# Kernel optimization log

Measured on AMD Instinct MI355X. Metric: run time of the kernel, lower is better.

Reference implementation:

```python
import jax, jax.numpy as jnp
import numpy as np

HID, HEADS = 1024, 16
HEAD_DIM = HID // HEADS
B, S = 4, 2048


def setup_inputs() -> dict:
    key = jax.random.key(0)
    ks = jax.random.split(key, 12)
    scale = 0.02
    inp = {
        "query": jax.random.normal(ks[0], (B, S, HID), jnp.float32),
        "key_in": jax.random.normal(ks[1], (B, S, HID), jnp.float32),
        "value": jax.random.normal(ks[2], (B, S, HID), jnp.float32),
        "mask": jnp.ones((B, 1, 1, S), jnp.int32),
        "Wq": jax.random.normal(ks[3], (HID, HID), jnp.float32) * scale,
        "bq": jnp.zeros((HID,), jnp.float32),
        "Wk": jax.random.normal(ks[4], (HID, HID), jnp.float32) * scale,
        "bk": jnp.zeros((HID,), jnp.float32),
        "Wv": jax.random.normal(ks[5], (HID, HID), jnp.float32) * scale,
        "bv": jnp.zeros((HID,), jnp.float32),
        "Wo": jax.random.normal(ks[6], (HID, HID), jnp.float32) * scale,
        "bo": jnp.zeros((HID,), jnp.float32),
    }
    return inp


def reference(query, key_in, value, mask, Wq, bq, Wk, bk, Wv, bv, Wo, bo):
    # Linear projections (torch Linear: x @ W.T + b)
    Q = query @ Wq.T + bq
    K = key_in @ Wk.T + bk
    V = value @ Wv.T + bv
    # [B, H, S, Dh]
    def split_heads(x):
        return x.reshape(B, -1, HEADS, HEAD_DIM).transpose(0, 2, 1, 3)
    Q, K, V = split_heads(Q), split_heads(K), split_heads(V)
    scale = jnp.sqrt(jnp.float32(HEAD_DIM))
    # multiplicative (scaled dot-product) attention: [B,H,Sq,Sk]
    energy = jnp.einsum("bhqd,bhkd->bhqk", Q, K) / scale
    energy = jnp.where(mask == 0, jnp.float32(-1e10), energy)
    attention = jax.nn.softmax(energy, axis=-1)
    x = jnp.einsum("bhqk,bhkd->bhqd", attention, V)  # dropout p=0
    x = x.transpose(0, 2, 1, 3).reshape(B, -1, HID)
    x = x @ Wo.T + bo
    return (x, attention)
```

## Files before the change

kernel.cpp:

```cpp
#include <hip/hip_runtime.h>
#include <hip/hip_bf16.h>
#include <stdint.h>
#include <stddef.h>

#define HID    1024
#define NHEADS 16
#define HD     64
#define BATCH  4
#define SEQ    2048

typedef __attribute__((ext_vector_type(8))) short short8;
typedef __attribute__((ext_vector_type(4))) short short4v;
typedef __attribute__((ext_vector_type(4))) float float4v;

static __device__ __forceinline__ short f2bf(float f) {
    unsigned u = __builtin_bit_cast(unsigned, f);
    u += 0x7fffu + ((u >> 16) & 1u);
    return (short)(u >> 16);
}

__global__ __launch_bounds__(256) void cvt_f32_bf16(const float* __restrict__ in,
                                                    short* __restrict__ out, int n4) {
    int i = blockIdx.x * 256 + threadIdx.x;
    if (i < n4) {
        float4v v = ((const float4v*)in)[i];
        short4v o;
        o[0] = f2bf(v[0]); o[1] = f2bf(v[1]); o[2] = f2bf(v[2]); o[3] = f2bf(v[3]);
        ((short4v*)out)[i] = o;
    }
}

template<int MODE, bool A_BF16>
__global__ __launch_bounds__(256) void gemm_kernel(const void* __restrict__ Aptr,
                                                   const short* __restrict__ Wb,
                                                   const float* __restrict__ bias,
                                                   void* __restrict__ outp) {
    const int lane = threadIdx.x & 63;
    const int w    = threadIdx.x >> 6;
    const int l15  = lane & 15;
    const int quad = lane >> 4;
    const int m0   = blockIdx.x * 64 + w * 16;
    const int n0   = blockIdx.y * 128;

    float4v acc[8];
#pragma unroll
    for (int i = 0; i < 8; i++)
#pragma unroll
        for (int j = 0; j < 4; j++) acc[i][j] = 0.0f;

    const int arow = m0 + l15;
    for (int ks = 0; ks < 1024; ks += 32) {
        const int koff = ks + quad * 8;
        short8 af;
        if (A_BF16) {
            const short* Ab = (const short*)Aptr;
            af = *(const short8*)(Ab + (size_t)arow * 1024 + koff);
        } else {
            const float* Af = (const float*)Aptr;
            float4v a0 = *(const float4v*)(Af + (size_t)arow * 1024 + koff);
            float4v a1 = *(const float4v*)(Af + (size_t)arow * 1024 + koff + 4);
            af[0] = f2bf(a0[0]); af[1] = f2bf(a0[1]); af[2] = f2bf(a0[2]); af[3] = f2bf(a0[3]);
            af[4] = f2bf(a1[0]); af[5] = f2bf(a1[1]); af[6] = f2bf(a1[2]); af[7] = f2bf(a1[3]);
        }
#pragma unroll
        for (int ns = 0; ns < 8; ns++) {
            const short8 bf = *(const short8*)(Wb + (size_t)(n0 + ns * 16 + l15) * 1024 + koff);
            acc[ns] = __builtin_amdgcn_mfma_f32_16x16x32_bf16(af, bf, acc[ns], 0, 0, 0);
        }
    }

#pragma unroll
    for (int ns = 0; ns < 8; ns++) {
        const int n = n0 + ns * 16 + l15;
        const float bv = bias[n];
        if (MODE == 0) {
            short* outb = (short*)outp;
#pragma unroll
            for (int r = 0; r < 4; r++) {
                const int m = m0 + quad * 4 + r;
                outb[(size_t)m * 1024 + n] = f2bf(acc[ns][r] + bv);
            }
        } else if (MODE == 1) {
            short* outb = (short*)outp;
            const int mb = m0 + quad * 4;
            const int b_ = mb >> 11, s_ = mb & 2047;
            const int h_ = n >> 6,  d_ = n & 63;
            short4v pk;
#pragma unroll
            for (int r = 0; r < 4; r++) pk[r] = f2bf(acc[ns][r] + bv);
            *(short4v*)(outb + ((size_t)((b_ * NHEADS + h_) * HD + d_)) * SEQ + s_) = pk;
        } else {
            float* outf = (float*)outp;
#pragma unroll
            for (int r = 0; r < 4; r++) {
                const int m = m0 + quad * 4 + r;
                outf[(size_t)m * 1024 + n] = acc[ns][r] + bv;
            }
        }
    }
}

__global__ __launch_bounds__(256) void attn_kernel(const short* __restrict__ Q,
                                                   const short* __restrict__ K,
                                                   const short* __restrict__ Vt,
                                                   const int* __restrict__ mask,
                                                   float* __restrict__ attn_out,
                                                   short* __restrict__ Xattn) {
    __shared__ short sP[4][16][40];

    const int lane = threadIdx.x & 63;
    const int w    = threadIdx.x >> 6;
    const int l15  = lane & 15;
    const int quad = lane >> 4;
    const int qblk = blockIdx.x & 31;
    const int bh   = blockIdx.x >> 5;
    const int b    = bh >> 4;
    const int h    = bh & 15;
    const int q0   = qblk * 64 + w * 16;

    const short* Qrow = Q + ((size_t)(b * SEQ + q0 + l15) * HID) + h * HD;
    const short8 aq0 = *(const short8*)(Qrow + quad * 8);
    const short8 aq1 = *(const short8*)(Qrow + 32 + quad * 8);

    const short* Kb   = K + (size_t)(b * SEQ) * HID + h * HD;
    const int*   mrow = mask + b * SEQ;
    const float  scale = 0.125f;

    float rs[4] = {0.f, 0.f, 0.f, 0.f};
    for (int n0 = 0; n0 < SEQ; n0 += 16) {
        const short* kr = Kb + (size_t)(n0 + l15) * HID + quad * 8;
        const short8 bk0 = *(const short8*)kr;
        const short8 bk1 = *(const short8*)(kr + 32);
        float4v e;
#pragma unroll
        for (int j = 0; j < 4; j++) e[j] = 0.0f;
        e = __builtin_amdgcn_mfma_f32_16x16x32_bf16(aq0, bk0, e, 0, 0, 0);
        e = __builtin_amdgcn_mfma_f32_16x16x32_bf16(aq1, bk1, e, 0, 0, 0);
        const int mv = mrow[n0 + l15];
#pragma unroll
        for (int r = 0; r < 4; r++) {
            float x = e[r] * scale;
            x = mv ? x : -1e10f;
            rs[r] += __expf(x);
        }
    }
#pragma unroll
    for (int r = 0; r < 4; r++) {
        float s = rs[r];
        s += __shfl_xor(s, 1, 64);
        s += __shfl_xor(s, 2, 64);
        s += __shfl_xor(s, 4, 64);
        s += __shfl_xor(s, 8, 64);
        rs[r] = 1.0f / s;
    }

    float4v oacc[4];
#pragma unroll
    for (int i = 0; i < 4; i++)
#pragma unroll
        for (int j = 0; j < 4; j++) oacc[i][j] = 0.0f;

    float* pout = attn_out + (size_t)(bh * SEQ + q0) * SEQ;
    const short* Vb = Vt + (size_t)bh * HD * SEQ;

    for (int n0 = 0; n0 < SEQ; n0 += 32) {
#pragma unroll
        for (int ns = 0; ns < 2; ns++) {
            const int nn = n0 + ns * 16;
            const short* kr = Kb + (size_t)(nn + l15) * HID + quad * 8;
            const short8 bk0 = *(const short8*)kr;
            const short8 bk1 = *(const short8*)(kr + 32);
            float4v e;
#pragma unroll
            for (int j = 0; j < 4; j++) e[j] = 0.0f;
            e = __builtin_amdgcn_mfma_f32_16x16x32_bf16(aq0, bk0, e, 0, 0, 0);
            e = __builtin_amdgcn_mfma_f32_16x16x32_bf16(aq1, bk1, e, 0, 0, 0);
            const int mv = mrow[nn + l15];
#pragma unroll
            for (int r = 0; r < 4; r++) {
                float x = e[r] * scale;
                x = mv ? x : -1e10f;
                const float p = __expf(x) * rs[r];
                const int m = quad * 4 + r;
                pout[(size_t)m * SEQ + nn + l15] = p;
                sP[w][m][ns * 16 + l15] = f2bf(p);
            }
        }
        __syncthreads();
        const short8 ap = *(const short8*)(&sP[w][l15][quad * 8]);
#pragma unroll
        for (int dn = 0; dn < 4; dn++) {
            const short8 bv = *(const short8*)(Vb + (size_t)(dn * 16 + l15) * SEQ + n0 + quad * 8);
            oacc[dn] = __builtin_amdgcn_mfma_f32_16x16x32_bf16(ap, bv, oacc[dn], 0, 0, 0);
        }
        __syncthreads();
    }

#pragma unroll
    for (int dn = 0; dn < 4; dn++)
#pragma unroll
        for (int r = 0; r < 4; r++) {
            const int m = quad * 4 + r;
            Xattn[(size_t)(b * SEQ + q0 + m) * HID + h * HD + dn * 16 + l15] = f2bf(oacc[dn][r]);
        }
}

extern "C" void kernel_launch(void* const* d_in, const int* in_sizes, int n_in,
                              void* d_out, int out_size, void* d_ws, size_t ws_size,
                              hipStream_t stream) {
    const float* query  = (const float*)d_in[0];
    const float* key_in = (const float*)d_in[1];
    const float* value  = (const float*)d_in[2];
    const int*   mask   = (const int*)d_in[3];
    const float* Wq = (const float*)d_in[4];
    const float* bq = (const float*)d_in[5];
    const float* Wk = (const float*)d_in[6];
    const float* bk = (const float*)d_in[7];
    const float* Wv = (const float*)d_in[8];
    const float* bv = (const float*)d_in[9];
    const float* Wo = (const float*)d_in[10];
    const float* bo = (const float*)d_in[11];

    char* ws = (char*)d_ws;
    const size_t MiB = 1024 * 1024;
    short* Wq_b = (short*)(ws + 0 * MiB);
    short* Wk_b = (short*)(ws + 2 * MiB);
    short* Wv_b = (short*)(ws + 4 * MiB);
    short* Wo_b = (short*)(ws + 6 * MiB);
    short* Qw   = (short*)(ws + 8 * MiB);
    short* Kw   = (short*)(ws + 24 * MiB);
    short* Vtw  = (short*)(ws + 40 * MiB);
    short* Xa   = (short*)(ws + 56 * MiB);

    const int wn4 = HID * HID / 4;
    cvt_f32_bf16<<<wn4 / 256, 256, 0, stream>>>(Wq, Wq_b, wn4);
    cvt_f32_bf16<<<wn4 / 256, 256, 0, stream>>>(Wk, Wk_b, wn4);
    cvt_f32_bf16<<<wn4 / 256, 256, 0, stream>>>(Wv, Wv_b, wn4);
    cvt_f32_bf16<<<wn4 / 256, 256, 0, stream>>>(Wo, Wo_b, wn4);

    dim3 gg(BATCH * SEQ / 64, HID / 128);
    gemm_kernel<0, false><<<gg, 256, 0, stream>>>(query,  Wq_b, bq, Qw);
    gemm_kernel<0, false><<<gg, 256, 0, stream>>>(key_in, Wk_b, bk, Kw);
    gemm_kernel<1, false><<<gg, 256, 0, stream>>>(value,  Wv_b, bv, Vtw);

    float* attn_out = (float*)d_out + (size_t)BATCH * SEQ * HID;
    attn_kernel<<<BATCH * NHEADS * (SEQ / 64), 256, 0, stream>>>(Qw, Kw, Vtw, mask, attn_out, Xa);

    gemm_kernel<2, true><<<gg, 256, 0, stream>>>(Xa, Wo_b, bo, d_out);
}
```

Baseline: 2.318 ms.

## Tile GEMMs through LDS, store Q/K head-major, prefetch K in attention

Replaces the register-only projection GEMM with a 128x128 LDS-tiled kernel. Tiles are filled by direct global-to-LDS loads, and block ids are swizzled for cache locality. Activations are first converted to bf16 in a separate pass, reusing a scratch buffer. Q and K are now written head-major so attention reads contiguous 64-element rows, and the attention loops software-prefetch the next K tile. Block barriers in the PV loop are replaced by a waitcnt, since each warp only uses its own sP slice. The cost is extra conversion kernels and an unpipelined single LDS buffer.

```diff
diff --git a/kernel.cpp b/kernel.cpp
--- a/kernel.cpp
+++ b/kernel.cpp
@@ -1,5 +1,4 @@
 #include <hip/hip_runtime.h>
-#include <hip/hip_bf16.h>
 #include <stdint.h>
 #include <stddef.h>
 
@@ -18,6 +17,11 @@
     u += 0x7fffu + ((u >> 16) & 1u);
     return (short)(u >> 16);
 }
+
+#define GLD_LDS16(g, l)                                        \
+    __builtin_amdgcn_global_load_lds(                          \
+        (__attribute__((address_space(1))) void*)(g),          \
+        (__attribute__((address_space(3))) void*)(l), 16, 0, 0)
 
 __global__ __launch_bounds__(256) void cvt_f32_bf16(const float* __restrict__ in,
                                                     short* __restrict__ out, int n4) {
@@ -30,71 +34,96 @@
     }
 }
 
-template<int MODE, bool A_BF16>
-__global__ __launch_bounds__(256) void gemm_kernel(const void* __restrict__ Aptr,
-                                                   const short* __restrict__ Wb,
-                                                   const float* __restrict__ bias,
-                                                   void* __restrict__ outp) {
-    const int lane = threadIdx.x & 63;
-    const int w    = threadIdx.x >> 6;
+template<int MODE>
+__global__ __launch_bounds__(256) void gemm_bf16(const short* __restrict__ A,
+                                                 const short* __restrict__ Wb,
+                                                 const float* __restrict__ bias,
+                                                 void* __restrict__ outp) {
+    __shared__ short As[128 * 32];
+    __shared__ short Bs[128 * 32];
+
+    const int id = blockIdx.x;
+    const int xt = (id & 7) * 8 + ((id >> 3) & 7);
+    const int yt = id >> 6;
+    const int m0 = xt * 128;
+    const int n0 = yt * 128;
+
+    const int t    = threadIdx.x;
+    const int lane = t & 63;
+    const int w    = t >> 6;
     const int l15  = lane & 15;
     const int quad = lane >> 4;
-    const int m0   = blockIdx.x * 64 + w * 16;
-    const int n0   = blockIdx.y * 128;
-
-    float4v acc[8];
-#pragma unroll
-    for (int i = 0; i < 8; i++)
-#pragma unroll
-        for (int j = 0; j < 4; j++) acc[i][j] = 0.0f;
-
-    const int arow = m0 + l15;
+    const int wm   = (w >> 1) * 64;
+    const int wn   = (w & 1) * 64;
+
+    float4v acc[4][4];
+#pragma unroll
+    for (int i = 0; i < 4; i++)
+#pragma unroll
+        for (int j = 0; j < 4; j++)
+#pragma unroll
+            for (int r = 0; r < 4; r++) acc[i][j][r] = 0.0f;
+
+    const int tr = t >> 2;
+    const int tc = (t & 3) * 8;
+    const short* Ag = A  + (size_t)(m0 + tr) * 1024 + tc;
+    const short* Wg = Wb + (size_t)(n0 + tr) * 1024 + tc;
+    short* a_dst = As + t * 8;
+    short* b_dst = Bs + t * 8;
+
     for (int ks = 0; ks < 1024; ks += 32) {
-        const int koff = ks + quad * 8;
-        short8 af;
-        if (A_BF16) {
-            const short* Ab = (const short*)Aptr;
-            af = *(const short8*)(Ab + (size_t)arow * 1024 + koff);
-        } else {
-            const float* Af = (const float*)Aptr;
-            float4v a0 = *(const float4v*)(Af + (size_t)arow * 1024 + koff);
-            float4v a1 = *(const float4v*)(Af + (size_t)arow * 1024 + koff + 4);
-            af[0] = f2bf(a0[0]); af[1] = f2bf(a0[1]); af[2] = f2bf(a0[2]); af[3] = f2bf(a0[3]);
-            af[4] = f2bf(a1[0]); af[5] = f2bf(a1[1]); af[6] = f2bf(a1[2]); af[7] = f2bf(a1[3]);
-        }
-#pragma unroll
-        for (int ns = 0; ns < 8; ns++) {
-            const short8 bf = *(const short8*)(Wb + (size_t)(n0 + ns * 16 + l15) * 1024 + koff);
-            acc[ns] = __builtin_amdgcn_mfma_f32_16x16x32_bf16(af, bf, acc[ns], 0, 0, 0);
-        }
-    }
-
-#pragma unroll
-    for (int ns = 0; ns < 8; ns++) {
-        const int n = n0 + ns * 16 + l15;
+        __syncthreads();
+        GLD_LDS16(Ag + ks,             a_dst);
+        GLD_LDS16(Ag + 64 * 1024 + ks, a_dst + 2048);
+        GLD_LDS16(Wg + ks,             b_dst);
+        GLD_LDS16(Wg + 64 * 1024 + ks, b_dst + 2048);
+        __syncthreads();
+
+        short8 af[4], bfr[4];
+#pragma unroll
+        for (int mi = 0; mi < 4; mi++)
+            af[mi] = *(const short8*)(As + (wm + mi * 16 + l15) * 32 + quad * 8);
+#pragma unroll
+        for (int ni = 0; ni < 4; ni++)
+            bfr[ni] = *(const short8*)(Bs + (wn + ni * 16 + l15) * 32 + quad * 8);
+#pragma unroll
+        for (int mi = 0; mi < 4; mi++)
+#pragma unroll
+            for (int ni = 0; ni < 4; ni++)
+                acc[mi][ni] = __builtin_amdgcn_mfma_f32_16x16x32_bf16(
+                    af[mi], bfr[ni], acc[mi][ni], 0, 0, 0);
+    }
+
+#pragma unroll
+    for (int ni = 0; ni < 4; ni++) {
+        const int n = n0 + wn + ni * 16 + l15;
         const float bv = bias[n];
-        if (MODE == 0) {
-            short* outb = (short*)outp;
-#pragma unroll
-            for (int r = 0; r < 4; r++) {
-                const int m = m0 + quad * 4 + r;
-                outb[(size_t)m * 1024 + n] = f2bf(acc[ns][r] + bv);
-            }
-        } else if (MODE == 1) {
-            short* outb = (short*)outp;
-            const int mb = m0 + quad * 4;
-            const int b_ = mb >> 11, s_ = mb & 2047;
-            const int h_ = n >> 6,  d_ = n & 63;
-            short4v pk;
-#pragma unroll
-            for (int r = 0; r < 4; r++) pk[r] = f2bf(acc[ns][r] + bv);
-            *(short4v*)(outb + ((size_t)((b_ * NHEADS + h_) * HD + d_)) * SEQ + s_) = pk;
-        } else {
-            float* outf = (float*)outp;
-#pragma unroll
-            for (int r = 0; r < 4; r++) {
-                const int m = m0 + quad * 4 + r;
-                outf[(size_t)m * 1024 + n] = acc[ns][r] + bv;
+#pragma unroll
+        for (int mi = 0; mi < 4; mi++) {
+            const int mb = m0 + wm + mi * 16 + quad * 4;
+            if (MODE == 3) {
+                short* ob = (short*)outp;
+                const int h_ = n >> 6, d_ = n & 63;
+                const int b_ = mb >> 11;
+#pragma unroll
+                for (int r = 0; r < 4; r++) {
+                    const int s_ = (mb + r) & 2047;
+                    ob[((size_t)(b_ * NHEADS + h_) * SEQ + s_) * HD + d_] =
+                        f2bf(acc[mi][ni][r] + bv);
+                }
+            } else if (MODE == 1) {
+                short* ob = (short*)outp;
+                const int h_ = n >> 6, d_ = n & 63;
+                const int b_ = mb >> 11, s_ = mb & 2047;
+                short4v pk;
+#pragma unroll
+                for (int r = 0; r < 4; r++) pk[r] = f2bf(acc[mi][ni][r] + bv);
+                *(short4v*)(ob + ((size_t)((b_ * NHEADS + h_) * HD + d_)) * SEQ + s_) = pk;
+            } else {
+                float* of = (float*)outp;
+#pragma unroll
+                for (int r = 0; r < 4; r++)
+                    of[(size_t)(mb + r) * 1024 + n] = acc[mi][ni][r] + bv;
             }
         }
     }
@@ -118,30 +147,38 @@
     const int h    = bh & 15;
     const int q0   = qblk * 64 + w * 16;
 
-    const short* Qrow = Q + ((size_t)(b * SEQ + q0 + l15) * HID) + h * HD;
+    const short* Qrow = Q + (size_t)(bh * SEQ + q0 + l15) * HD;
     const short8 aq0 = *(const short8*)(Qrow + quad * 8);
     const short8 aq1 = *(const short8*)(Qrow + 32 + quad * 8);
 
-    const short* Kb   = K + (size_t)(b * SEQ) * HID + h * HD;
+    const short* Kb   = K + (size_t)bh * SEQ * HD;
     const int*   mrow = mask + b * SEQ;
     const float  scale = 0.125f;
 
     float rs[4] = {0.f, 0.f, 0.f, 0.f};
-    for (int n0 = 0; n0 < SEQ; n0 += 16) {
-        const short* kr = Kb + (size_t)(n0 + l15) * HID + quad * 8;
-        const short8 bk0 = *(const short8*)kr;
-        const short8 bk1 = *(const short8*)(kr + 32);
-        float4v e;
-#pragma unroll
-        for (int j = 0; j < 4; j++) e[j] = 0.0f;
-        e = __builtin_amdgcn_mfma_f32_16x16x32_bf16(aq0, bk0, e, 0, 0, 0);
-        e = __builtin_amdgcn_mfma_f32_16x16x32_bf16(aq1, bk1, e, 0, 0, 0);
-        const int mv = mrow[n0 + l15];
-#pragma unroll
-        for (int r = 0; r < 4; r++) {
-            float x = e[r] * scale;
-            x = mv ? x : -1e10f;
-            rs[r] += __expf(x);
+    {
+        const short* kp = Kb + (size_t)l15 * HD;
+        short8 nk0 = *(const short8*)(kp + quad * 8);
+        short8 nk1 = *(const short8*)(kp + 32 + quad * 8);
+        int nmv = mrow[l15];
+        for (int n0 = 0; n0 < SEQ; n0 += 16) {
+            const short8 ck0 = nk0, ck1 = nk1;
+            const int cmv = nmv;
+            if (n0 + 16 < SEQ) {
+                const short* kn = Kb + (size_t)(n0 + 16 + l15) * HD;
+                nk0 = *(const short8*)(kn + quad * 8);
+                nk1 = *(const short8*)(kn + 32 + quad * 8);
+                nmv = mrow[n0 + 16 + l15];
+            }
+            float4v e = {0.f, 0.f, 0.f, 0.f};
+            e = __builtin_amdgcn_mfma_f32_16x16x32_bf16(aq0, ck0, e, 0, 0, 0);
+            e = __builtin_amdgcn_mfma_f32_16x16x32_bf16(aq1, ck1, e, 0, 0, 0);
+#pragma unroll
+            for (int r = 0; r < 4; r++) {
+                float x = e[r] * scale;
+                x = cmv ? x : -1e10f;
+                rs[r] += __expf(x);
+            }
         }
     }
 #pragma unroll
@@ -163,45 +200,77 @@
     float* pout = attn_out + (size_t)(bh * SEQ + q0) * SEQ;
     const short* Vb = Vt + (size_t)bh * HD * SEQ;
 
+    short8 k00, k01, k10, k11;
+    int mv0, mv1;
+    {
+        const short* k0p = Kb + (size_t)l15 * HD;
+        const short* k1p = Kb + (size_t)(16 + l15) * HD;
+        k00 = *(const short8*)(k0p + quad * 8);
+        k01 = *(const short8*)(k0p + 32 + quad * 8);
+        k10 = *(const short8*)(k1p + quad * 8);
+        k11 = *(const short8*)(k1p + 32 + quad * 8);
+        mv0 = mrow[l15];
+        mv1 = mrow[16 + l15];
+    }
+
     for (int n0 = 0; n0 < SEQ; n0 += 32) {
-#pragma unroll
-        for (int ns = 0; ns < 2; ns++) {
-            const int nn = n0 + ns * 16;
-            const short* kr = Kb + (size_t)(nn + l15) * HID + quad * 8;
-            const short8 bk0 = *(const short8*)kr;
-            const short8 bk1 = *(const short8*)(kr + 32);
-            float4v e;
-#pragma unroll
-            for (int j = 0; j < 4; j++) e[j] = 0.0f;
-            e = __builtin_amdgcn_mfma_f32_16x16x32_bf16(aq0, bk0, e, 0, 0, 0);
-            e = __builtin_amdgcn_mfma_f32_16x16x32_bf16(aq1, bk1, e, 0, 0, 0);
-            const int mv = mrow[nn + l15];
-#pragma unroll
-            for (int r = 0; r < 4; r++) {
-                float x = e[r] * scale;
-                x = mv ? x : -1e10f;
-                const float p = __expf(x) * rs[r];
-                const int m = quad * 4 + r;
-                pout[(size_t)m * SEQ + nn + l15] = p;
-                sP[w][m][ns * 16 + l15] = f2bf(p);
-            }
-        }
-        __syncthreads();
-        const short8 ap = *(const short8*)(&sP[w][l15][quad * 8]);
-#pragma unroll
-        for (int dn = 0; dn < 4; dn++) {
-            const short8 bv = *(const short8*)(Vb + (size_t)(dn * 16 + l15) * SEQ + n0 + quad * 8);
-            oacc[dn] = __builtin_amdgcn_mfma_f32_16x16x32_bf16(ap, bv, oacc[dn], 0, 0, 0);
-        }
-        __syncthreads();
-    }
-
-#pragma unroll
-    for (int dn = 0; dn < 4; dn++)
+        const short8 c00 = k00, c01 = k01, c10 = k10, c11 = k11;
+        const int cm0 = mv0, cm1 = mv1;
+
+        short8 bv[4];
+#pragma unroll
+        for (int dn = 0; dn < 4; dn++)
+            bv[dn] = *(const short8*)(Vb + (size_t)(dn * 16 + l15) * SEQ + n0 + quad * 8);
+
+        if (n0 + 32 < SEQ) {
+            const short* k0p = Kb + (size_t)(n0 + 32 + l15) * HD;
+            const short* k1p = Kb + (size_t)(n0 + 48 + l15) * HD;
+            k00 = *(const short8*)(k0p + quad * 8);
+            k01 = *(const short8*)(k0p + 32 + quad * 8);
+            k10 = *(const short8*)(k1p + quad * 8);
+            k11 = *(const short8*)(k1p + 32 + quad * 8);
+            mv0 = mrow[n0 + 32 + l15];
+            mv1 = mrow[n0 + 48 + l15];
+        }
+
+        float4v e0 = {0.f, 0.f, 0.f, 0.f};
+        float4v e1 = {0.f, 0.f, 0.f, 0.f};
+        e0 = __builtin_amdgcn_mfma_f32_16x16x32_bf16(aq0, c00, e0, 0, 0, 0);
+        e0 = __builtin_amdgcn_mfma_f32_16x16x32_bf16(aq1, c01, e0, 0, 0, 0);
+        e1 = __builtin_amdgcn_mfma_f32_16x16x32_bf16(aq0, c10, e1, 0, 0, 0);
+        e1 = __builtin_amdgcn_mfma_f32_16x16x32_bf16(aq1, c11, e1, 0, 0, 0);
+
 #pragma unroll
         for (int r = 0; r < 4; r++) {
             const int m = quad * 4 + r;
-            Xattn[(size_t)(b * SEQ + q0 + m) * HID + h * HD + dn * 16 + l15] = f2bf(oacc[dn][r]);
+            float x0 = e0[r] * scale;
+            x0 = cm0 ? x0 : -1e10f;
+            const float p0 = __expf(x0) * rs[r];
+            pout[(size_t)m * SEQ + n0 + l15] = p0;
+            sP[w][m][l15] = f2bf(p0);
+            float x1 = e1[r] * scale;
+            x1 = cm1 ? x1 : -1e10f;
+            const float p1 = __expf(x1) * rs[r];
+            pout[(size_t)m * SEQ + n0 + 16 + l15] = p1;
+            sP[w][m][16 + l15] = f2bf(p1);
+        }
+
+        asm volatile("s_waitcnt lgkmcnt(0)" ::: "memory");
+        __builtin_amdgcn_sched_barrier(0);
+
+        const short8 ap = *(const short8*)(&sP[w][l15][quad * 8]);
+#pragma unroll
+        for (int dn = 0; dn < 4; dn++)
+            oacc[dn] = __builtin_amdgcn_mfma_f32_16x16x32_bf16(ap, bv[dn], oacc[dn], 0, 0, 0);
+    }
+
+#pragma unroll
+    for (int dn = 0; dn < 4; dn++)
+#pragma unroll
+        for (int r = 0; r < 4; r++) {
+            const int m = quad * 4 + r;
+            Xattn[(size_t)(b * SEQ + q0 + m) * HID + h * HD + dn * 16 + l15] =
+                f2bf(oacc[dn][r]);
         }
 }
 
@@ -231,6 +300,7 @@
     short* Kw   = (short*)(ws + 24 * MiB);
     short* Vtw  = (short*)(ws + 40 * MiB);
     short* Xa   = (short*)(ws + 56 * MiB);
+    short* T    = Xa;
 
     const int wn4 = HID * HID / 4;
     cvt_f32_bf16<<<wn4 / 256, 256, 0, stream>>>(Wq, Wq_b, wn4);
@@ -238,13 +308,19 @@
     cvt_f32_bf16<<<wn4 / 256, 256, 0, stream>>>(Wv, Wv_b, wn4);
     cvt_f32_bf16<<<wn4 / 256, 256, 0, stream>>>(Wo, Wo_b, wn4);
 
-    dim3 gg(BATCH * SEQ / 64, HID / 128);
-    gemm_kernel<0, false><<<gg, 256, 0, stream>>>(query,  Wq_b, bq, Qw);
-    gemm_kernel<0, false><<<gg, 256, 0, stream>>>(key_in, Wk_b, bk, Kw);
-    gemm_kernel<1, false><<<gg, 256, 0, stream>>>(value,  Wv_b, bv, Vtw);
+    const int an4 = BATCH * SEQ * HID / 4;
+    const int GEMM_GRID = (BATCH * SEQ / 128) * (HID / 128);
+
+    cvt_f32_bf16<<<an4 / 256, 256, 0, stream>>>(query, T, an4);
+    gemm_bf16<3><<<GEMM_GRID, 256, 0, stream>>>(T, Wq_b, bq, Qw);
+    cvt_f32_bf16<<<an4 / 256, 256, 0, stream>>>(key_in, T, an4);
+    gemm_bf16<3><<<GEMM_GRID, 256, 0, stream>>>(T, Wk_b, bk, Kw);
+    cvt_f32_bf16<<<an4 / 256, 256, 0, stream>>>(value, T, an4);
+    gemm_bf16<1><<<GEMM_GRID, 256, 0, stream>>>(T, Wv_b, bv, Vtw);
 
     float* attn_out = (float*)d_out + (size_t)BATCH * SEQ * HID;
-    attn_kernel<<<BATCH * NHEADS * (SEQ / 64), 256, 0, stream>>>(Qw, Kw, Vtw, mask, attn_out, Xa);
-
-    gemm_kernel<2, true><<<gg, 256, 0, stream>>>(Xa, Wo_b, bo, d_out);
-}
+    attn_kernel<<<BATCH * NHEADS * (SEQ / 64), 256, 0, stream>>>(Qw, Kw, Vtw, mask,
+                                                                 attn_out, Xa);
+
+    gemm_bf16<2><<<GEMM_GRID, 256, 0, stream>>>(Xa, Wo_b, bo, d_out);
+}
```

Measured after the change: 1.900 ms. -18.1%, faster.
